# Performance work log

Hardware: AMD Instinct MI355X
Metric: run time of the kernel (lower is better)

The kernel has to match this reference:

```python
import jax, jax.numpy as jnp
import numpy as np

N_HEAD = 16
N_EMBD = 1024
HEAD_DIM = N_EMBD // N_HEAD


def setup_inputs() -> dict:
    key = jax.random.key(0)
    k1, k2, k3 = jax.random.split(key, 3)
    B, T, C = 2, 2048, N_EMBD
    x = jax.random.normal(k1, (B, T, C), dtype=jnp.float32)
    # nn.Linear weights: (out_features, in_features)
    W_attn = jax.random.normal(k2, (3 * C, C), dtype=jnp.float32) * 0.02
    W_proj = jax.random.normal(k3, (C, C), dtype=jnp.float32) * 0.02
    return {"x": x, "W_attn": W_attn, "W_proj": W_proj}


def reference(x, W_attn, W_proj):
    B, T, C = x.shape
    h, hd = N_HEAD, HEAD_DIM
    # c_attn: x @ W^T, then split into q, k, v
    qkv = jnp.einsum('btc,dc->btd', x, W_attn)  # [B, T, 3C]
    q, k, v = jnp.split(qkv, 3, axis=-1)
    # [B, T, C] -> [B, h, T, hd]
    q = q.reshape(B, T, h, hd).transpose(0, 2, 1, 3)
    k = k.reshape(B, T, h, hd).transpose(0, 2, 1, 3)
    v = v.reshape(B, T, h, hd).transpose(0, 2, 1, 3)
    # NOTE: no 1/sqrt(hd) scaling in the original module
    logits = jnp.einsum('bhnk,bhmk->bhnm', q, k)  # [B, h, T, T]
    causal = jnp.tril(jnp.ones((T, T), dtype=bool))  # [T, T]
    logits = jnp.where(causal[None, None, :, :], logits, -jnp.inf)
    weights = jax.nn.softmax(logits, axis=-1)
    O = jnp.einsum('bhnm,bhmv->bhnv', weights, v)  # [B, h, T, hd]
    # Original: einsum('bhnv,hdv->bnd', O, c_proj.weight) with weight viewed as (h, d, v)
    Wp = W_proj.reshape(h, C, hd)
    Y = jnp.einsum('bhnv,hdv->bnd', O, Wp)  # [B, T, C]
    return Y
```

## Files before the change

kernel.cpp:

```cpp
#include <hip/hip_runtime.h>
#include <stdint.h>
#include <math.h>

#define B_    2
#define T_    2048
#define C_    1024
#define H_    16
#define D_    64
#define MTOT  4096
#define NQKV  3072
#define KDIM  1024

#define LOG2E 1.4426950408889634f

typedef short short8 __attribute__((ext_vector_type(8)));
typedef float f32x4  __attribute__((ext_vector_type(4)));

__device__ __forceinline__ uint16_t f2b(float f) {
    union { float f; uint32_t u; } x; x.f = f;
    uint32_t u = x.u;
    return (uint16_t)((u + 0x7FFFu + ((u >> 16) & 1u)) >> 16);
}
__device__ __forceinline__ uint32_t packb2(float a, float b) {
    union { float f; uint32_t u; } x, y; x.f = a; y.f = b;
    return ((x.u + 0x8000u) >> 16) | ((y.u + 0x8000u) & 0xffff0000u);
}
__device__ __forceinline__ uint32_t packb2_rne(float a, float b) {
    return (uint32_t)f2b(a) | ((uint32_t)f2b(b) << 16);
}
__device__ __forceinline__ float fexp2(float x) {
#if __has_builtin(__builtin_amdgcn_exp2f)
    return __builtin_amdgcn_exp2f(x);
#else
    return exp2f(x);
#endif
}

__global__ __launch_bounds__(256) void cast_all(const float* __restrict__ x,
                                                const float* __restrict__ wa,
                                                uint16_t* __restrict__ xb,
                                                uint16_t* __restrict__ wab,
                                                int n4x, int n4w) {
    int i = blockIdx.x * blockDim.x + threadIdx.x;
    const float* src; uint16_t* dst; int j;
    if (i < n4x) { src = x; dst = xb; j = i; }
    else { j = i - n4x; if (j >= n4w) return; src = wa; dst = wab; }
    float4 v = ((const float4*)src)[j];
    ushort4 o;
    o.x = f2b(v.x); o.y = f2b(v.y); o.z = f2b(v.z); o.w = f2b(v.w);
    ((ushort4*)dst)[j] = o;
}

__global__ __launch_bounds__(256) void cast_wp(const float* __restrict__ wp,
                                               uint16_t* __restrict__ wt) {
    int i = blockIdx.x * blockDim.x + threadIdx.x;
    int j4 = (i & 255) * 4;
    int d  = i >> 8;
    int h = j4 >> 6, v = j4 & 63;
    float4 val = *(const float4*)(wp + h * 65536 + d * 64 + v);
    ushort4 o;
    o.x = f2b(val.x); o.y = f2b(val.y); o.z = f2b(val.z); o.w = f2b(val.w);
    *(ushort4*)(wt + d * 1024 + j4) = o;
}

__global__ __launch_bounds__(256, 3) void gemm_qkv(const uint16_t* __restrict__ A,
                                                   const uint16_t* __restrict__ Bw,
                                                   uint16_t* __restrict__ qkvb) {
    __shared__ __align__(16) uint16_t As[128 * 64];
    __shared__ __align__(16) uint16_t Bs[128 * 64];

    int tid = threadIdx.x;
    int w = tid >> 6, lane = tid & 63;
    int qd = lane >> 4, ln = lane & 15;
    int lnx = ln & 7;
    int rowBase = blockIdx.y * 128;
    int colBase = blockIdx.x * 128;
    int mw = (w >> 1) * 64, nw = (w & 1) * 64;

    int srow = tid >> 3;
    int pchunk = tid & 7;
    int gchunk = pchunk ^ (srow & 7);

    const uint16_t* ga = A  + (size_t)(rowBase + srow) * KDIM + gchunk * 8;
    const uint16_t* gb = Bw + (size_t)(colBase + srow) * KDIM + gchunk * 8;
    uint16_t* la = &As[srow * 64 + pchunk * 8];
    uint16_t* lb = &Bs[srow * 64 + pchunk * 8];

    short8 pa[4], pb[4];
#pragma unroll
    for (int m = 0; m < 4; m++) {
        pa[m] = *(const short8*)(ga + (size_t)m * 32 * KDIM);
        pb[m] = *(const short8*)(gb + (size_t)m * 32 * KDIM);
    }

    f32x4 acc[4][4] = {};
    for (int s = 0; s < 16; s++) {
#pragma unroll
        for (int m = 0; m < 4; m++) {
            *(short8*)(la + m * 32 * 64) = pa[m];
            *(short8*)(lb + m * 32 * 64) = pb[m];
        }
        __syncthreads();
        if (s < 15) {
            int k0 = (s + 1) * 64;
#pragma unroll
            for (int m = 0; m < 4; m++) {
                pa[m] = *(const short8*)(ga + k0 + (size_t)m * 32 * KDIM);
                pb[m] = *(const short8*)(gb + k0 + (size_t)m * 32 * KDIM);
            }
        }
#pragma unroll
        for (int ks = 0; ks < 2; ks++) {
            int p = (ks * 4 + qd) ^ lnx;
            short8 a[4], b[4];
#pragma unroll
            for (int i = 0; i < 4; i++) {
                a[i] = *(const short8*)&As[(mw + i * 16 + ln) * 64 + p * 8];
                b[i] = *(const short8*)&Bs[(nw + i * 16 + ln) * 64 + p * 8];
            }
#pragma unroll
            for (int i = 0; i < 4; i++)
#pragma unroll
                for (int j = 0; j < 4; j++)
                    acc[i][j] = __builtin_amdgcn_mfma_f32_16x16x32_bf16(a[i], b[j], acc[i][j], 0, 0, 0);
        }
        __syncthreads();
    }

#pragma unroll
    for (int i = 0; i < 4; i++) {
#pragma unroll
        for (int j = 0; j < 4; j++) {
            int gcol = colBase + nw + j * 16 + ln;
            int which = gcol >> 10;
            int rem = gcol & 1023;
            int h = rem >> 6, d = rem & 63;
            float sc = (which == 0) ? LOG2E : 1.0f;
#pragma unroll
            for (int r = 0; r < 4; r++) {
                int grow = rowBase + mw + i * 16 + qd * 4 + r;
                int bb = grow >> 11, t = grow & 2047;
                uint16_t val = f2b(acc[i][j][r] * sc);
                if (which == 2) {
                    qkvb[(size_t)2 * 4194304 + (((size_t)(bb * H_ + h) * D_) + d) * T_ + t] = val;
                } else {
                    qkvb[(size_t)which * 4194304 + (((size_t)(bb * H_ + h) * T_) + t) * D_ + d] = val;
                }
            }
        }
    }
}

__global__ __launch_bounds__(128) void attn(const uint16_t* __restrict__ qkvb,
                                            uint16_t* __restrict__ oc) {
    union ShU {
        uint16_t Pl[2][64][72];
        struct { f32x4 Cb[16][64]; float Lb[64][4]; } c;
    };
    __shared__ __align__(16) ShU sh;

    int tid = threadIdx.x;
    int w = tid >> 6, lane = tid & 63;
    int qd = lane >> 4, ln = lane & 15;
    int bid = blockIdx.x;
    int qt = 31 - (bid >> 5);
    int bh = bid & 31;
    int qbase = qt * 64;
    int ntiles = qt + 1;

    const uint16_t* Q  = qkvb + (size_t)bh * T_ * D_;
    const uint16_t* K  = Q + 4194304;
    const uint16_t* Vt = qkvb + (size_t)2 * 4194304 + (size_t)bh * D_ * T_;

    short8 bq[4][2];
#pragma unroll
    for (int jq = 0; jq < 4; jq++)
#pragma unroll
        for (int ks = 0; ks < 2; ks++)
            bq[jq][ks] = *(const short8*)(Q + (size_t)(qbase + jq * 16 + ln) * D_ + ks * 32 + qd * 8);

    f32x4 ot[4][4] = {};
    float l_part[4] = {};

    for (int kt = w; kt < ntiles; kt += 2) {
        short8 ak[4][2], av[4][2];
#pragma unroll
        for (int it = 0; it < 4; it++)
#pragma unroll
            for (int ks = 0; ks < 2; ks++)
                ak[it][ks] = *(const short8*)(K + (size_t)(kt * 64 + it * 16 + ln) * D_ + ks * 32 + qd * 8);
#pragma unroll
        for (int id = 0; id < 4; id++)
#pragma unroll
            for (int ks = 0; ks < 2; ks++)
                av[id][ks] = *(const short8*)(Vt + (size_t)(id * 16 + ln) * T_ + kt * 64 + ks * 32 + qd * 8);

        bool diag = (kt == qt);
#pragma unroll
        for (int it = 0; it < 4; it++) {
            f32x4 stt[4] = {};
#pragma unroll
            for (int ks = 0; ks < 2; ks++)
#pragma unroll
                for (int jq = 0; jq < 4; jq++)
                    stt[jq] = __builtin_amdgcn_mfma_f32_16x16x32_bf16(ak[it][ks], bq[jq][ks], stt[jq], 0, 0, 0);
            if (diag) {
#pragma unroll
                for (int jq = 0; jq < 4; jq++)
#pragma unroll
                    for (int r = 0; r < 4; r++) {
                        int t = it * 16 + qd * 4 + r;
                        int q = jq * 16 + ln;
                        if (t > q) stt[jq][r] = -1.0e30f;
                    }
            }
#pragma unroll
            for (int jq = 0; jq < 4; jq++) {
                float p0 = fexp2(stt[jq][0]);
                float p1 = fexp2(stt[jq][1]);
                float p2 = fexp2(stt[jq][2]);
                float p3 = fexp2(stt[jq][3]);
                l_part[jq] += (p0 + p1) + (p2 + p3);
                uint2 pk;
                pk.x = packb2(p0, p1);
                pk.y = packb2(p2, p3);
                *(uint2*)&sh.Pl[w][jq * 16 + ln][it * 16 + qd * 4] = pk;
            }
        }

        short8 bp[4][2];
#pragma unroll
        for (int jq = 0; jq < 4; jq++)
#pragma unroll
            for (int ks = 0; ks < 2; ks++)
                bp[jq][ks] = *(const short8*)&sh.Pl[w][jq * 16 + ln][ks * 32 + qd * 8];

#pragma unroll
        for (int ks = 0; ks < 2; ks++)
#pragma unroll
            for (int id = 0; id < 4; id++)
#pragma unroll
                for (int jq = 0; jq < 4; jq++)
                    ot[id][jq] = __builtin_amdgcn_mfma_f32_16x16x32_bf16(av[id][ks], bp[jq][ks], ot[id][jq], 0, 0, 0);
    }

    __syncthreads();
    if (w == 1) {
#pragma unroll
        for (int id = 0; id < 4; id++)
#pragma unroll
            for (int jq = 0; jq < 4; jq++)
                sh.c.Cb[id * 4 + jq][lane] = ot[id][jq];
        f32x4 lp = { l_part[0], l_part[1], l_part[2], l_part[3] };
        *(f32x4*)&sh.c.Lb[lane][0] = lp;
    }
    __syncthreads();
    if (w == 0) {
#pragma unroll
        for (int id = 0; id < 4; id++)
#pragma unroll
            for (int jq = 0; jq < 4; jq++)
                ot[id][jq] += sh.c.Cb[id * 4 + jq][lane];
        f32x4 lo = *(const f32x4*)&sh.c.Lb[lane][0];
        float rl[4];
#pragma unroll
        for (int jq = 0; jq < 4; jq++) {
            float s = l_part[jq] + lo[jq];
            s += __shfl_xor(s, 16);
            s += __shfl_xor(s, 32);
            rl[jq] = 1.0f / s;
        }
        int b = bh >> 4, h = bh & 15;
#pragma unroll
        for (int id = 0; id < 4; id++)
#pragma unroll
            for (int jq = 0; jq < 4; jq++) {
                float v0 = ot[id][jq][0] * rl[jq];
                float v1 = ot[id][jq][1] * rl[jq];
                float v2 = ot[id][jq][2] * rl[jq];
                float v3 = ot[id][jq][3] * rl[jq];
                uint2 pk;
                pk.x = packb2_rne(v0, v1);
                pk.y = packb2_rne(v2, v3);
                int q = qbase + jq * 16 + ln;
                *(uint2*)&oc[(size_t)(b * T_ + q) * C_ + h * 64 + id * 16 + qd * 4] = pk;
            }
    }
}

__global__ __launch_bounds__(256, 3) void gemm_out(const uint16_t* __restrict__ A,
                                                   const uint16_t* __restrict__ Bw,
                                                   float* __restrict__ out) {
    __shared__ __align__(16) uint16_t As[128 * 64];
    __shared__ __align__(16) uint16_t Bs[64 * 64];

    int tid = threadIdx.x;
    int w = tid >> 6, lane = tid & 63;
    int qd = lane >> 4, ln = lane & 15;
    int lnx = ln & 7;
    int rowBase = blockIdx.y * 128;
    int colBase = blockIdx.x * 64;
    int mw = (w >> 1) * 64, nw = (w & 1) * 32;

    int srow = tid >> 3;
    int pchunk = tid & 7;
    int gchunk = pchunk ^ (srow & 7);

    const uint16_t* ga = A  + (size_t)(rowBase + srow) * KDIM + gchunk * 8;
    const uint16_t* gb = Bw + (size_t)(colBase + srow) * KDIM + gchunk * 8;
    uint16_t* la = &As[srow * 64 + pchunk * 8];
    uint16_t* lb = &Bs[srow * 64 + pchunk * 8];

    short8 pa[4], pb[2];
#pragma unroll
    for (int m = 0; m < 4; m++)
        pa[m] = *(const short8*)(ga + (size_t)m * 32 * KDIM);
#pragma unroll
    for (int m = 0; m < 2; m++)
        pb[m] = *(const short8*)(gb + (size_t)m * 32 * KDIM);

    f32x4 acc[4][2] = {};
    for (int s = 0; s < 16; s++) {
#pragma unroll
        for (int m = 0; m < 4; m++)
            *(short8*)(la + m * 32 * 64) = pa[m];
#pragma unroll
        for (int m = 0; m < 2; m++)
            *(short8*)(lb + m * 32 * 64) = pb[m];
        __syncthreads();
        if (s < 15) {
            int k0 = (s + 1) * 64;
#pragma unroll
            for (int m = 0; m < 4; m++)
                pa[m] = *(const short8*)(ga + k0 + (size_t)m * 32 * KDIM);
#pragma unroll
            for (int m = 0; m < 2; m++)
                pb[m] = *(const short8*)(gb + k0 + (size_t)m * 32 * KDIM);
        }
#pragma unroll
        for (int ks = 0; ks < 2; ks++) {
            int p = (ks * 4 + qd) ^ lnx;
            short8 a[4], b[2];
#pragma unroll
            for (int i = 0; i < 4; i++)
                a[i] = *(const short8*)&As[(mw + i * 16 + ln) * 64 + p * 8];
#pragma unroll
            for (int j = 0; j < 2; j++)
                b[j] = *(const short8*)&Bs[(nw + j * 16 + ln) * 64 + p * 8];
#pragma unroll
            for (int i = 0; i < 4; i++)
#pragma unroll
                for (int j = 0; j < 2; j++)
                    acc[i][j] = __builtin_amdgcn_mfma_f32_16x16x32_bf16(a[i], b[j], acc[i][j], 0, 0, 0);
        }
        __syncthreads();
    }

#pragma unroll
    for (int i = 0; i < 4; i++)
#pragma unroll
        for (int j = 0; j < 2; j++)
#pragma unroll
            for (int r = 0; r < 4; r++) {
                int grow = rowBase + mw + i * 16 + qd * 4 + r;
                int gcol = colBase + nw + j * 16 + ln;
                out[(size_t)grow * 1024 + gcol] = acc[i][j][r];
            }
}

extern "C" void kernel_launch(void* const* d_in, const int* in_sizes, int n_in,
                              void* d_out, int out_size, void* d_ws, size_t ws_size,
                              hipStream_t stream) {
    const float* x  = (const float*)d_in[0];
    const float* Wa = (const float*)d_in[1];
    const float* Wp = (const float*)d_in[2];
    float* out = (float*)d_out;

    uint16_t* ws   = (uint16_t*)d_ws;
    uint16_t* xb   = ws;
    uint16_t* Wab  = xb + 4194304;
    uint16_t* Wtb  = Wab + 3145728;
    uint16_t* qkvb = Wtb + 1048576;
    uint16_t* ob   = qkvb + (size_t)3 * 4194304;

    cast_all<<<7168, 256, 0, stream>>>(x, Wa, xb, Wab, 4194304 / 4, 3145728 / 4);
    cast_wp<<<1024, 256, 0, stream>>>(Wp, Wtb);
    gemm_qkv<<<dim3(24, 32), 256, 0, stream>>>(xb, Wab, qkvb);
    attn<<<1024, 128, 0, stream>>>(qkvb, ob);
    gemm_out<<<dim3(16, 32), 256, 0, stream>>>(ob, Wtb, out);
}
```

Before: 173.7 us.

## Pair causal query tiles per block and split key tiles across four waves

```diff
diff --git a/kernel.cpp b/kernel.cpp
--- a/kernel.cpp
+++ b/kernel.cpp
@@ -151,11 +151,11 @@
     }
 }
 
-__global__ __launch_bounds__(128) void attn(const uint16_t* __restrict__ qkvb,
-                                            uint16_t* __restrict__ oc) {
+__global__ __launch_bounds__(256, 2) void attn(const uint16_t* __restrict__ qkvb,
+                                               uint16_t* __restrict__ oc) {
     union ShU {
-        uint16_t Pl[2][64][72];
-        struct { f32x4 Cb[16][64]; float Lb[64][4]; } c;
+        uint16_t Pl[4][64][72];
+        struct { f32x4 Cb[2][16][64]; float Lb[2][64][4]; } c;
     };
     __shared__ __align__(16) ShU sh;
 
@@ -163,128 +163,161 @@
     int w = tid >> 6, lane = tid & 63;
     int qd = lane >> 4, ln = lane & 15;
     int bid = blockIdx.x;
-    int qt = 31 - (bid >> 5);
+    int pr = bid >> 5;
     int bh = bid & 31;
-    int qbase = qt * 64;
-    int ntiles = qt + 1;
-
-    const uint16_t* Q  = qkvb + (size_t)bh * T_ * D_;
-    const uint16_t* K  = Q + 4194304;
+
+    const uint16_t* Q0 = qkvb + (size_t)bh * T_ * D_;
+    const uint16_t* K  = Q0 + 4194304;
     const uint16_t* Vt = qkvb + (size_t)2 * 4194304 + (size_t)bh * D_ * T_;
-
-    short8 bq[4][2];
-#pragma unroll
-    for (int jq = 0; jq < 4; jq++)
-#pragma unroll
-        for (int ks = 0; ks < 2; ks++)
-            bq[jq][ks] = *(const short8*)(Q + (size_t)(qbase + jq * 16 + ln) * D_ + ks * 32 + qd * 8);
-
-    f32x4 ot[4][4] = {};
-    float l_part[4] = {};
-
-    for (int kt = w; kt < ntiles; kt += 2) {
-        short8 ak[4][2], av[4][2];
-#pragma unroll
-        for (int it = 0; it < 4; it++)
+    int b = bh >> 4, h = bh & 15;
+
+#pragma unroll 1
+    for (int ph = 0; ph < 2; ph++) {
+        int qt = ph ? pr : (31 - pr);
+        int qbase = qt * 64;
+        int nt = qt + 1;
+
+        short8 bq[4][2];
+#pragma unroll
+        for (int jq = 0; jq < 4; jq++)
 #pragma unroll
             for (int ks = 0; ks < 2; ks++)
-                ak[it][ks] = *(const short8*)(K + (size_t)(kt * 64 + it * 16 + ln) * D_ + ks * 32 + qd * 8);
-#pragma unroll
-        for (int id = 0; id < 4; id++)
+                bq[jq][ks] = *(const short8*)(Q0 + (size_t)(qbase + jq * 16 + ln) * D_ + ks * 32 + qd * 8);
+
+        f32x4 ot[4][4] = {};
+        float l_part[4] = {};
+
+        for (int kt = w; kt < nt; kt += 4) {
+            short8 ak[4][2], av[4][2];
+#pragma unroll
+            for (int it = 0; it < 4; it++)
+#pragma unroll
+                for (int ks = 0; ks < 2; ks++)
+                    ak[it][ks] = *(const short8*)(K + (size_t)(kt * 64 + it * 16 + ln) * D_ + ks * 32 + qd * 8);
+#pragma unroll
+            for (int id = 0; id < 4; id++)
+#pragma unroll
+                for (int ks = 0; ks < 2; ks++)
+                    av[id][ks] = *(const short8*)(Vt + (size_t)(id * 16 + ln) * T_ + kt * 64 + ks * 32 + qd * 8);
+
+            bool diag = (kt == qt);
+#pragma unroll
+            for (int it = 0; it < 4; it++) {
+                f32x4 stt[4] = {};
+                __builtin_amdgcn_s_setprio(1);
+#pragma unroll
+                for (int ks = 0; ks < 2; ks++)
+#pragma unroll
+                    for (int jq = 0; jq < 4; jq++)
+                        stt[jq] = __builtin_amdgcn_mfma_f32_16x16x32_bf16(ak[it][ks], bq[jq][ks], stt[jq], 0, 0, 0);
+                __builtin_amdgcn_s_setprio(0);
+                if (diag) {
+#pragma unroll
+                    for (int jq = 0; jq < 4; jq++)
+#pragma unroll
+                        for (int r = 0; r < 4; r++) {
+                            int t = it * 16 + qd * 4 + r;
+                            int q = jq * 16 + ln;
+                            if (t > q) stt[jq][r] = -1.0e30f;
+                        }
+                }
+#pragma unroll
+                for (int jq = 0; jq < 4; jq++) {
+                    float p0 = fexp2(stt[jq][0]);
+                    float p1 = fexp2(stt[jq][1]);
+                    float p2 = fexp2(stt[jq][2]);
+                    float p3 = fexp2(stt[jq][3]);
+                    l_part[jq] += (p0 + p1) + (p2 + p3);
+                    uint2 pk;
+                    pk.x = packb2(p0, p1);
+                    pk.y = packb2(p2, p3);
+                    *(uint2*)&sh.Pl[w][jq * 16 + ln][it * 16 + qd * 4] = pk;
+                }
+            }
+
+            short8 bp[4][2];
+#pragma unroll
+            for (int jq = 0; jq < 4; jq++)
+#pragma unroll
+                for (int ks = 0; ks < 2; ks++)
+                    bp[jq][ks] = *(const short8*)&sh.Pl[w][jq * 16 + ln][ks * 32 + qd * 8];
+
+            __builtin_amdgcn_s_setprio(1);
 #pragma unroll
             for (int ks = 0; ks < 2; ks++)
-                av[id][ks] = *(const short8*)(Vt + (size_t)(id * 16 + ln) * T_ + kt * 64 + ks * 32 + qd * 8);
-
-        bool diag = (kt == qt);
-#pragma unroll
-        for (int it = 0; it < 4; it++) {
-            f32x4 stt[4] = {};
-#pragma unroll
-            for (int ks = 0; ks < 2; ks++)
+#pragma unroll
+                for (int id = 0; id < 4; id++)
+#pragma unroll
+                    for (int jq = 0; jq < 4; jq++)
+                        ot[id][jq] = __builtin_amdgcn_mfma_f32_16x16x32_bf16(av[id][ks], bp[jq][ks], ot[id][jq], 0, 0, 0);
+            __builtin_amdgcn_s_setprio(0);
+        }
+
+        __syncthreads();
+        if (w >= 2) {
+            int slot = w - 2;
+#pragma unroll
+            for (int id = 0; id < 4; id++)
 #pragma unroll
                 for (int jq = 0; jq < 4; jq++)
-                    stt[jq] = __builtin_amdgcn_mfma_f32_16x16x32_bf16(ak[it][ks], bq[jq][ks], stt[jq], 0, 0, 0);
-            if (diag) {
+                    sh.c.Cb[slot][id * 4 + jq][lane] = ot[id][jq];
+            f32x4 lp = { l_part[0], l_part[1], l_part[2], l_part[3] };
+            *(f32x4*)&sh.c.Lb[slot][lane][0] = lp;
+        }
+        __syncthreads();
+        if (w < 2) {
+#pragma unroll
+            for (int id = 0; id < 4; id++)
 #pragma unroll
                 for (int jq = 0; jq < 4; jq++)
-#pragma unroll
-                    for (int r = 0; r < 4; r++) {
-                        int t = it * 16 + qd * 4 + r;
-                        int q = jq * 16 + ln;
-                        if (t > q) stt[jq][r] = -1.0e30f;
-                    }
-            }
+                    ot[id][jq] += sh.c.Cb[w][id * 4 + jq][lane];
+            f32x4 lo = *(const f32x4*)&sh.c.Lb[w][lane][0];
+#pragma unroll
+            for (int jq = 0; jq < 4; jq++)
+                l_part[jq] += lo[jq];
+        }
+        __syncthreads();
+        if (w == 1) {
+#pragma unroll
+            for (int id = 0; id < 4; id++)
+#pragma unroll
+                for (int jq = 0; jq < 4; jq++)
+                    sh.c.Cb[0][id * 4 + jq][lane] = ot[id][jq];
+            f32x4 lp = { l_part[0], l_part[1], l_part[2], l_part[3] };
+            *(f32x4*)&sh.c.Lb[0][lane][0] = lp;
+        }
+        __syncthreads();
+        if (w == 0) {
+#pragma unroll
+            for (int id = 0; id < 4; id++)
+#pragma unroll
+                for (int jq = 0; jq < 4; jq++)
+                    ot[id][jq] += sh.c.Cb[0][id * 4 + jq][lane];
+            f32x4 lo = *(const f32x4*)&sh.c.Lb[0][lane][0];
+            float rl[4];
 #pragma unroll
             for (int jq = 0; jq < 4; jq++) {
-                float p0 = fexp2(stt[jq][0]);
-                float p1 = fexp2(stt[jq][1]);
-                float p2 = fexp2(stt[jq][2]);
-                float p3 = fexp2(stt[jq][3]);
-                l_part[jq] += (p0 + p1) + (p2 + p3);
-                uint2 pk;
-                pk.x = packb2(p0, p1);
-                pk.y = packb2(p2, p3);
-                *(uint2*)&sh.Pl[w][jq * 16 + ln][it * 16 + qd * 4] = pk;
-            }
-        }
-
-        short8 bp[4][2];
-#pragma unroll
-        for (int jq = 0; jq < 4; jq++)
-#pragma unroll
-            for (int ks = 0; ks < 2; ks++)
-                bp[jq][ks] = *(const short8*)&sh.Pl[w][jq * 16 + ln][ks * 32 + qd * 8];
-
-#pragma unroll
-        for (int ks = 0; ks < 2; ks++)
-#pragma unroll
-            for (int id = 0; id < 4; id++)
-#pragma unroll
-                for (int jq = 0; jq < 4; jq++)
-                    ot[id][jq] = __builtin_amdgcn_mfma_f32_16x16x32_bf16(av[id][ks], bp[jq][ks], ot[id][jq], 0, 0, 0);
-    }
-
-    __syncthreads();
-    if (w == 1) {
-#pragma unroll
-        for (int id = 0; id < 4; id++)
-#pragma unroll
-            for (int jq = 0; jq < 4; jq++)
-                sh.c.Cb[id * 4 + jq][lane] = ot[id][jq];
-        f32x4 lp = { l_part[0], l_part[1], l_part[2], l_part[3] };
-        *(f32x4*)&sh.c.Lb[lane][0] = lp;
-    }
-    __syncthreads();
-    if (w == 0) {
-#pragma unroll
-        for (int id = 0; id < 4; id++)
-#pragma unroll
-            for (int jq = 0; jq < 4; jq++)
-                ot[id][jq] += sh.c.Cb[id * 4 + jq][lane];
-        f32x4 lo = *(const f32x4*)&sh.c.Lb[lane][0];
-        float rl[4];
-#pragma unroll
-        for (int jq = 0; jq < 4; jq++) {
-            float s = l_part[jq] + lo[jq];
-            s += __shfl_xor(s, 16);
-            s += __shfl_xor(s, 32);
-            rl[jq] = 1.0f / s;
-        }
-        int b = bh >> 4, h = bh & 15;
-#pragma unroll
-        for (int id = 0; id < 4; id++)
-#pragma unroll
-            for (int jq = 0; jq < 4; jq++) {
-                float v0 = ot[id][jq][0] * rl[jq];
-                float v1 = ot[id][jq][1] * rl[jq];
-                float v2 = ot[id][jq][2] * rl[jq];
-                float v3 = ot[id][jq][3] * rl[jq];
-                uint2 pk;
-                pk.x = packb2_rne(v0, v1);
-                pk.y = packb2_rne(v2, v3);
-                int q = qbase + jq * 16 + ln;
-                *(uint2*)&oc[(size_t)(b * T_ + q) * C_ + h * 64 + id * 16 + qd * 4] = pk;
-            }
+                float s = l_part[jq] + lo[jq];
+                s += __shfl_xor(s, 16);
+                s += __shfl_xor(s, 32);
+                rl[jq] = 1.0f / s;
+            }
+#pragma unroll
+            for (int id = 0; id < 4; id++)
+#pragma unroll
+                for (int jq = 0; jq < 4; jq++) {
+                    float v0 = ot[id][jq][0] * rl[jq];
+                    float v1 = ot[id][jq][1] * rl[jq];
+                    float v2 = ot[id][jq][2] * rl[jq];
+                    float v3 = ot[id][jq][3] * rl[jq];
+                    uint2 pk;
+                    pk.x = packb2_rne(v0, v1);
+                    pk.y = packb2_rne(v2, v3);
+                    int q = qbase + jq * 16 + ln;
+                    *(uint2*)&oc[(size_t)(b * T_ + q) * C_ + h * 64 + id * 16 + qd * 4] = pk;
+                }
+        }
+        __syncthreads();
     }
 }
 
@@ -386,6 +419,6 @@
     cast_all<<<7168, 256, 0, stream>>>(x, Wa, xb, Wab, 4194304 / 4, 3145728 / 4);
     cast_wp<<<1024, 256, 0, stream>>>(Wp, Wtb);
     gemm_qkv<<<dim3(24, 32), 256, 0, stream>>>(xb, Wab, qkvb);
-    attn<<<1024, 128, 0, stream>>>(qkvb, ob);
+    attn<<<512, 256, 0, stream>>>(qkvb, ob);
     gemm_out<<<dim3(16, 32), 256, 0, stream>>>(ob, Wtb, out);
 }
```

New measurement: 179.6 us. 1.03x slower.

## Restructure attention into 8-wave blocks with shared K/V tiles and paired causal strips

Applied to the files above, without the earlier changes.

```diff
diff --git a/kernel.cpp b/kernel.cpp
--- a/kernel.cpp
+++ b/kernel.cpp
@@ -151,141 +151,141 @@
     }
 }
 
-__global__ __launch_bounds__(128) void attn(const uint16_t* __restrict__ qkvb,
-                                            uint16_t* __restrict__ oc) {
-    union ShU {
-        uint16_t Pl[2][64][72];
-        struct { f32x4 Cb[16][64]; float Lb[64][4]; } c;
-    };
-    __shared__ __align__(16) ShU sh;
+
+#define STRIP(QS, BQ, OT, LSUM)                                              \
+    if (kt * 64 <= (QS) + 15) {                                              \
+        bool needm = (kt * 64 + 63 > (QS));                                  \
+        f32x4 stt[4];                                                        \
+        __builtin_amdgcn_s_setprio(1);                                       \
+        _Pragma("unroll")                                                    \
+        for (int it = 0; it < 4; it++) {                                     \
+            f32x4 z = {};                                                    \
+            z = __builtin_amdgcn_mfma_f32_16x16x32_bf16(ak[it][0], (BQ)[0], z, 0, 0, 0); \
+            z = __builtin_amdgcn_mfma_f32_16x16x32_bf16(ak[it][1], (BQ)[1], z, 0, 0, 0); \
+            stt[it] = z;                                                     \
+        }                                                                    \
+        __builtin_amdgcn_s_setprio(0);                                       \
+        if (needm) {                                                         \
+            _Pragma("unroll")                                                \
+            for (int it = 0; it < 4; it++)                                   \
+                _Pragma("unroll")                                            \
+                for (int r = 0; r < 4; r++) {                                \
+                    int t = kt * 64 + it * 16 + qd * 4 + r;                  \
+                    if (t > (QS) + ln) stt[it][r] = -1.0e30f;                \
+                }                                                            \
+        }                                                                    \
+        _Pragma("unroll")                                                    \
+        for (int it = 0; it < 4; it++) {                                     \
+            float p0 = fexp2(stt[it][0]);                                    \
+            float p1 = fexp2(stt[it][1]);                                    \
+            float p2 = fexp2(stt[it][2]);                                    \
+            float p3 = fexp2(stt[it][3]);                                    \
+            (LSUM) += (p0 + p1) + (p2 + p3);                                 \
+            uint2 pk2;                                                       \
+            pk2.x = packb2(p0, p1);                                          \
+            pk2.y = packb2(p2, p3);                                          \
+            *(uint2*)&Pl[w][ln][it * 16 + qd * 4] = pk2;                     \
+        }                                                                    \
+        short8 bp0 = *(const short8*)&Pl[w][ln][qd * 8];                     \
+        short8 bp1 = *(const short8*)&Pl[w][ln][32 + qd * 8];                \
+        __builtin_amdgcn_s_setprio(1);                                       \
+        _Pragma("unroll")                                                    \
+        for (int id = 0; id < 4; id++) {                                     \
+            (OT)[id] = __builtin_amdgcn_mfma_f32_16x16x32_bf16(av[id][0], bp0, (OT)[id], 0, 0, 0); \
+            (OT)[id] = __builtin_amdgcn_mfma_f32_16x16x32_bf16(av[id][1], bp1, (OT)[id], 0, 0, 0); \
+        }                                                                    \
+        __builtin_amdgcn_s_setprio(0);                                       \
+    }
+
+#define EPI(QS, OT, LSUM)                                                    \
+    {                                                                        \
+        float ssum = (LSUM);                                                 \
+        ssum += __shfl_xor(ssum, 16);                                        \
+        ssum += __shfl_xor(ssum, 32);                                        \
+        float rl = 1.0f / ssum;                                              \
+        int q = (QS) + ln;                                                   \
+        _Pragma("unroll")                                                    \
+        for (int id = 0; id < 4; id++) {                                     \
+            float v0 = (OT)[id][0] * rl;                                     \
+            float v1 = (OT)[id][1] * rl;                                     \
+            float v2 = (OT)[id][2] * rl;                                     \
+            float v3 = (OT)[id][3] * rl;                                     \
+            uint2 pk2;                                                       \
+            pk2.x = packb2_rne(v0, v1);                                      \
+            pk2.y = packb2_rne(v2, v3);                                      \
+            *(uint2*)&oc[(size_t)(b * T_ + q) * C_ + h * 64 + id * 16 + qd * 4] = pk2; \
+        }                                                                    \
+    }
+
+__global__ __launch_bounds__(512, 2) void attn(const uint16_t* __restrict__ qkvb,
+                                               uint16_t* __restrict__ oc) {
+    __shared__ __align__(16) uint16_t Ks[2][64 * 64];
+    __shared__ __align__(16) uint16_t Vs[2][64 * 64];
+    __shared__ __align__(16) uint16_t Pl[8][16][72];
 
     int tid = threadIdx.x;
     int w = tid >> 6, lane = tid & 63;
     int qd = lane >> 4, ln = lane & 15;
+    int lnx = ln & 7;
     int bid = blockIdx.x;
-    int qt = 31 - (bid >> 5);
+    int j = bid >> 5;
     int bh = bid & 31;
-    int qbase = qt * 64;
-    int ntiles = qt + 1;
-
-    const uint16_t* Q  = qkvb + (size_t)bh * T_ * D_;
-    const uint16_t* K  = Q + 4194304;
+    int b = bh >> 4, h = bh & 15;
+
+    const uint16_t* Q0 = qkvb + (size_t)bh * T_ * D_;
+    const uint16_t* K  = Q0 + 4194304;
     const uint16_t* Vt = qkvb + (size_t)2 * 4194304 + (size_t)bh * D_ * T_;
 
-    short8 bq[4][2];
-#pragma unroll
-    for (int jq = 0; jq < 4; jq++)
-#pragma unroll
-        for (int ks = 0; ks < 2; ks++)
-            bq[jq][ks] = *(const short8*)(Q + (size_t)(qbase + jq * 16 + ln) * D_ + ks * 32 + qd * 8);
-
-    f32x4 ot[4][4] = {};
-    float l_part[4] = {};
-
-    for (int kt = w; kt < ntiles; kt += 2) {
+    int qsA = j * 128 + w * 16;
+    int qsB = (15 - j) * 128 + w * 16;
+    int nt  = 32 - 2 * j;
+
+    short8 bqA[2], bqB[2];
+#pragma unroll
+    for (int ks = 0; ks < 2; ks++) {
+        bqA[ks] = *(const short8*)(Q0 + (size_t)(qsA + ln) * D_ + ks * 32 + qd * 8);
+        bqB[ks] = *(const short8*)(Q0 + (size_t)(qsB + ln) * D_ + ks * 32 + qd * 8);
+    }
+
+    int srow = tid >> 3;
+    int pch = tid & 7;
+    int gch = pch ^ (srow & 7);
+    const uint16_t* gk = K  + (size_t)srow * D_ + gch * 8;
+    const uint16_t* gv = Vt + (size_t)srow * T_ + gch * 8;
+    int lofs = srow * 64 + pch * 8;
+
+    short8 pk = *(const short8*)gk;
+    short8 pv = *(const short8*)gv;
+
+    f32x4 otA[4] = {}, otB[4] = {};
+    float lA = 0.f, lB = 0.f;
+
+    int c = 0;
+    for (int kt = 0; kt < nt; kt++) {
+        *(short8*)&Ks[c][lofs] = pk;
+        *(short8*)&Vs[c][lofs] = pv;
+        __syncthreads();
+        if (kt + 1 < nt) {
+            pk = *(const short8*)(gk + (size_t)(kt + 1) * 64 * D_);
+            pv = *(const short8*)(gv + (size_t)(kt + 1) * 64);
+        }
         short8 ak[4][2], av[4][2];
 #pragma unroll
-        for (int it = 0; it < 4; it++)
-#pragma unroll
-            for (int ks = 0; ks < 2; ks++)
-                ak[it][ks] = *(const short8*)(K + (size_t)(kt * 64 + it * 16 + ln) * D_ + ks * 32 + qd * 8);
-#pragma unroll
-        for (int id = 0; id < 4; id++)
-#pragma unroll
-            for (int ks = 0; ks < 2; ks++)
-                av[id][ks] = *(const short8*)(Vt + (size_t)(id * 16 + ln) * T_ + kt * 64 + ks * 32 + qd * 8);
-
-        bool diag = (kt == qt);
-#pragma unroll
-        for (int it = 0; it < 4; it++) {
-            f32x4 stt[4] = {};
-#pragma unroll
-            for (int ks = 0; ks < 2; ks++)
-#pragma unroll
-                for (int jq = 0; jq < 4; jq++)
-                    stt[jq] = __builtin_amdgcn_mfma_f32_16x16x32_bf16(ak[it][ks], bq[jq][ks], stt[jq], 0, 0, 0);
-            if (diag) {
-#pragma unroll
-                for (int jq = 0; jq < 4; jq++)
-#pragma unroll
-                    for (int r = 0; r < 4; r++) {
-                        int t = it * 16 + qd * 4 + r;
-                        int q = jq * 16 + ln;
-                        if (t > q) stt[jq][r] = -1.0e30f;
-                    }
-            }
-#pragma unroll
-            for (int jq = 0; jq < 4; jq++) {
-                float p0 = fexp2(stt[jq][0]);
-                float p1 = fexp2(stt[jq][1]);
-                float p2 = fexp2(stt[jq][2]);
-                float p3 = fexp2(stt[jq][3]);
-                l_part[jq] += (p0 + p1) + (p2 + p3);
-                uint2 pk;
-                pk.x = packb2(p0, p1);
-                pk.y = packb2(p2, p3);
-                *(uint2*)&sh.Pl[w][jq * 16 + ln][it * 16 + qd * 4] = pk;
-            }
-        }
-
-        short8 bp[4][2];
-#pragma unroll
-        for (int jq = 0; jq < 4; jq++)
-#pragma unroll
-            for (int ks = 0; ks < 2; ks++)
-                bp[jq][ks] = *(const short8*)&sh.Pl[w][jq * 16 + ln][ks * 32 + qd * 8];
-
-#pragma unroll
-        for (int ks = 0; ks < 2; ks++)
-#pragma unroll
-            for (int id = 0; id < 4; id++)
-#pragma unroll
-                for (int jq = 0; jq < 4; jq++)
-                    ot[id][jq] = __builtin_amdgcn_mfma_f32_16x16x32_bf16(av[id][ks], bp[jq][ks], ot[id][jq], 0, 0, 0);
-    }
-
-    __syncthreads();
-    if (w == 1) {
-#pragma unroll
-        for (int id = 0; id < 4; id++)
-#pragma unroll
-            for (int jq = 0; jq < 4; jq++)
-                sh.c.Cb[id * 4 + jq][lane] = ot[id][jq];
-        f32x4 lp = { l_part[0], l_part[1], l_part[2], l_part[3] };
-        *(f32x4*)&sh.c.Lb[lane][0] = lp;
-    }
-    __syncthreads();
-    if (w == 0) {
-#pragma unroll
-        for (int id = 0; id < 4; id++)
-#pragma unroll
-            for (int jq = 0; jq < 4; jq++)
-                ot[id][jq] += sh.c.Cb[id * 4 + jq][lane];
-        f32x4 lo = *(const f32x4*)&sh.c.Lb[lane][0];
-        float rl[4];
-#pragma unroll
-        for (int jq = 0; jq < 4; jq++) {
-            float s = l_part[jq] + lo[jq];
-            s += __shfl_xor(s, 16);
-            s += __shfl_xor(s, 32);
-            rl[jq] = 1.0f / s;
-        }
-        int b = bh >> 4, h = bh & 15;
-#pragma unroll
-        for (int id = 0; id < 4; id++)
-#pragma unroll
-            for (int jq = 0; jq < 4; jq++) {
-                float v0 = ot[id][jq][0] * rl[jq];
-                float v1 = ot[id][jq][1] * rl[jq];
-                float v2 = ot[id][jq][2] * rl[jq];
-                float v3 = ot[id][jq][3] * rl[jq];
-                uint2 pk;
-                pk.x = packb2_rne(v0, v1);
-                pk.y = packb2_rne(v2, v3);
-                int q = qbase + jq * 16 + ln;
-                *(uint2*)&oc[(size_t)(b * T_ + q) * C_ + h * 64 + id * 16 + qd * 4] = pk;
-            }
-    }
+        for (int ks = 0; ks < 2; ks++) {
+            int p8 = ((ks * 4 + qd) ^ lnx) * 8;
+#pragma unroll
+            for (int it = 0; it < 4; it++) {
+                ak[it][ks] = *(const short8*)&Ks[c][(it * 16 + ln) * 64 + p8];
+                av[it][ks] = *(const short8*)&Vs[c][(it * 16 + ln) * 64 + p8];
+            }
+        }
+        STRIP(qsA, bqA, otA, lA);
+        STRIP(qsB, bqB, otB, lB);
+        c ^= 1;
+    }
+
+    EPI(qsA, otA, lA);
+    EPI(qsB, otB, lB);
 }
 
 __global__ __launch_bounds__(256, 3) void gemm_out(const uint16_t* __restrict__ A,
@@ -386,6 +386,6 @@
     cast_all<<<7168, 256, 0, stream>>>(x, Wa, xb, Wab, 4194304 / 4, 3145728 / 4);
     cast_wp<<<1024, 256, 0, stream>>>(Wp, Wtb);
     gemm_qkv<<<dim3(24, 32), 256, 0, stream>>>(xb, Wab, qkvb);
-    attn<<<1024, 128, 0, stream>>>(qkvb, ob);
+    attn<<<256, 512, 0, stream>>>(qkvb, ob);
     gemm_out<<<dim3(16, 32), 256, 0, stream>>>(ob, Wtb, out);
 }
```

Result: faster. 168.0 us (-3.3%).
